# Kernel tuning notes

Hardware: AMD Instinct MI355X
Metric: run time of the kernel (lower is better)

The kernel has to match this reference:

```python
import jax, jax.numpy as jnp
import numpy as np
from jax import lax

B, T, D_IN, H1, H2 = 200, 500, 300, 256, 300


def _lstm(x, Wih, Whh, bih, bhh, H):
    """PyTorch-convention LSTM (gate order i,f,g,o), zero init state.
    x: [B,T,Din] -> outputs [B,T,H]."""
    b = x.shape[0]
    # Precompute input contribution for all timesteps: [B,T,4H]
    xg = jnp.einsum('bti,gi->btg', x, Wih) + bih + bhh

    def step(carry, xg_t):
        h, c = carry
        g = xg_t + h @ Whh.T  # [B,4H]
        i = jax.nn.sigmoid(g[:, :H])
        f = jax.nn.sigmoid(g[:, H:2 * H])
        gg = jnp.tanh(g[:, 2 * H:3 * H])
        o = jax.nn.sigmoid(g[:, 3 * H:])
        c = f * c + i * gg
        h = o * jnp.tanh(c)
        return (h, c), h

    init = (jnp.zeros((b, H), x.dtype), jnp.zeros((b, H), x.dtype))
    _, hs = lax.scan(step, init, jnp.swapaxes(xg, 0, 1))  # [T,B,H]
    return jnp.swapaxes(hs, 0, 1)


def _uniform(key, shape, H):
    s = 1.0 / np.sqrt(H)
    return jax.random.uniform(key, shape, jnp.float32, -s, s)


def setup_inputs() -> dict:
    key = jax.random.key(0)
    ks = jax.random.split(key, 10)
    x = jax.random.normal(ks[0], (B, T, D_IN), jnp.float32)
    lengths = jax.random.randint(ks[1], (B,), 1, T + 1, jnp.int32)
    return {
        'x': x,
        'lengths': lengths,
        'Wih1': _uniform(ks[2], (4 * H1, D_IN), H1),
        'Whh1': _uniform(ks[3], (4 * H1, H1), H1),
        'bih1': _uniform(ks[4], (4 * H1,), H1),
        'bhh1': _uniform(ks[5], (4 * H1,), H1),
        'Wih2': _uniform(ks[6], (4 * H2, H1), H2),
        'Whh2': _uniform(ks[7], (4 * H2, H2), H2),
        'bih2': _uniform(ks[8], (4 * H2,), H2),
        'bhh2': _uniform(ks[9], (4 * H2,), H2),
    }


def reference(x, lengths, Wih1, Whh1, bih1, bhh1, Wih2, Whh2, bih2, bhh2):
    # lstm1 on packed sequence == causal per-sample LSTM + zero out padding
    out1 = _lstm(x, Wih1, Whh1, bih1, bhh1, H1)  # [B,T,H1]
    mask = (jnp.arange(T)[None, :] < lengths[:, None])  # [B,T]
    out1 = out1 * mask[:, :, None].astype(out1.dtype)   # pad_packed zeros
    # vectorized "last valid timestep" gather (replaces host-sync loop)
    idx = (lengths - 1).astype(jnp.int32)[:, None, None]
    h_value = jnp.take_along_axis(out1, idx, axis=1)[:, 0, :]  # [B,H1]
    # lstm2 runs over the full padded (zeroed) sequence, as in the original
    out2 = _lstm(out1, Wih2, Whh2, bih2, bhh2, H2)  # [B,T,H2]
    return (out2, h_value)
```

## Files before the change

kernel.cpp:

```cpp
#include <hip/hip_runtime.h>
#include <math.h>

#define TSEQ 500
#define BQ   200
#define DIN  300
#define H1   256
#define H2   300
#define K1   556
#define KP   576
#define H1P  256
#define H2P  304
#define BQC  25
#define LB1  8
#define LBT  18
#define NBLK 144

#define H1SLOT (BQ*H1P)
#define H2SLOT (BQ*H2P)

#define WS_H1   0
#define WS_H2   307200
#define WS_C1   672000
#define WS_C2   876800
#define WS_FLG  1132800
#define WS_MSET 1133824

typedef __attribute__((ext_vector_type(8))) short short8;
typedef __attribute__((ext_vector_type(4))) float f32x4;
typedef unsigned long long u64;

__device__ __forceinline__ float sigf(float v){ return 1.0f/(1.0f+__expf(-v)); }
__device__ __forceinline__ float tanhf_(float v){
    v = fminf(15.0f, fmaxf(-15.0f, v));
    float e = __expf(2.0f*v);
    return (e-1.0f)/(e+1.0f);
}
__device__ __forceinline__ unsigned short f2bf(float f){
    unsigned int xx = __builtin_bit_cast(unsigned int, f);
    xx = (xx + 0x7FFFu + ((xx>>16)&1u)) >> 16;
    return (unsigned short)xx;
}
__device__ __forceinline__ u64 ld8_sys(const void* p){
    return __hip_atomic_load((const u64*)p, __ATOMIC_RELAXED, __HIP_MEMORY_SCOPE_SYSTEM);
}
__device__ __forceinline__ void pub8(u64* p, u64 v){
    u64 old = __hip_atomic_exchange(p, v, __ATOMIC_RELAXED, __HIP_MEMORY_SCOPE_SYSTEM);
    asm volatile("" :: "v"(old));
}

union U16B { short8 s8; u64 u[2]; unsigned short us[8]; };
union U8B  { u64 u; unsigned short us[4]; };

__global__ __launch_bounds__(512, 2)
void lstm_mfma(const float* __restrict__ x, const int* __restrict__ lengths,
               const float* __restrict__ Wih1, const float* __restrict__ Whh1,
               const float* __restrict__ bih1, const float* __restrict__ bhh1,
               const float* __restrict__ Wih2, const float* __restrict__ Whh2,
               const float* __restrict__ bih2, const float* __restrict__ bhh2,
               float* __restrict__ out, char* __restrict__ wsb,
               int it_begin, int it_end, int coop)
{
    __shared__ unsigned short Al[32*KP];
    __shared__ float gl[128*33];
    __shared__ float bias[128];
    __shared__ int lenl[32];

    const int tid = threadIdx.x;
    const int bid = blockIdx.x;
    const int mc  = bid & 7;
    const int lbi = bid >> 3;
    const bool l1 = lbi < LB1;
    const int ub  = (l1 ? lbi : lbi - LB1) * 32;
    const int Hl  = l1 ? H1 : H2;

    unsigned short* h1s = (unsigned short*)(wsb + WS_H1);
    unsigned short* h2s = (unsigned short*)(wsb + WS_H2);
    float* c1 = (float*)(wsb + WS_C1);
    float* c2 = (float*)(wsb + WS_C2);
    int* flg = (int*)(wsb + WS_FLG + mc*128);

    const int wave = tid >> 6, lane = tid & 63;
    const int fr = lane & 15, fg = lane >> 4;
    const int sw = fr & 7;

    short8 wreg[18];
    {
        const int row = wave*16 + fr;
        const int u = row >> 2, g = row & 3;
        const int unit = ub + u;
        const bool vr = unit < Hl;
        const long grow = (long)g*Hl + unit;
        #pragma unroll
        for (int ks = 0; ks < 18; ++ks){
            unsigned short v8[8];
            #pragma unroll
            for (int j = 0; j < 8; ++j){
                int k = ks*32 + fg*8 + j;
                float v = 0.0f;
                if (vr && k < K1){
                    if (l1) v = (k < H1) ? Whh1[grow*H1 + k] : Wih1[grow*DIN + (k - H1)];
                    else    v = (k < H1) ? Wih2[grow*H1 + k] : Whh2[grow*H2 + (k - H1)];
                }
                v8[j] = f2bf(v);
            }
            wreg[ks] = *(short8*)v8;
        }
    }
    if (tid < 128){
        int u = tid >> 2, g = tid & 3, unit = ub + u;
        bias[tid] = (unit < Hl)
            ? ((l1?bih1:bih2)[g*Hl+unit] + (l1?bhh1:bhh2)[g*Hl+unit]) : 0.0f;
    }
    if (tid < 32) lenl[tid] = (tid < BQC) ? lengths[mc*BQC + tid] : 0;

    const unsigned short* arow0 = &Al[fr*KP];
    const unsigned short* arow1 = &Al[(16+fr)*KP];
    const int bg_e = mc*BQC + lane;

    float creg[4] = {0.f, 0.f, 0.f, 0.f};
    if (!coop && lane < 32){
        float* cs = l1 ? c1 : c2;
        #pragma unroll
        for (int i2 = 0; i2 < 4; ++i2) creg[i2] = cs[(ub + wave*4 + i2)*BQ + bg_e];
    }

    __syncthreads();

    for (int it = it_begin; it < it_end; ++it){
        const bool active = l1 ? (it < TSEQ) : (it >= 1);
        const int t = l1 ? it : it - 1;

        if (active && l1){
            #pragma unroll
            for (int i = 0; i < 3; ++i){
                int e = tid + i*512;
                if (e < 1280){
                    int bl = e/40, kcx = 32 + e - (e/40)*40;
                    U16B v; v.u[0] = 0; v.u[1] = 0;
                    if (bl < BQC && kcx <= 69){
                        int bg = mc*BQC + bl;
                        const float* xp = x + ((size_t)bg*TSEQ + t)*DIN + (kcx*8 - 256);
                        float4 f0 = *(const float4*)xp;
                        v.us[0]=f2bf(f0.x); v.us[1]=f2bf(f0.y); v.us[2]=f2bf(f0.z); v.us[3]=f2bf(f0.w);
                        if (kcx <= 68){
                            float4 f1 = *(const float4*)(xp + 4);
                            v.us[4]=f2bf(f1.x); v.us[5]=f2bf(f1.y); v.us[6]=f2bf(f1.z); v.us[7]=f2bf(f1.w);
                        }
                    }
                    *(short8*)&Al[bl*KP + ((kcx ^ (bl&7))<<3)] = v.s8;
                }
            }
        }

        if (coop && it > it_begin && tid < LBT){
            int tgt = l1 ? (tid < LB1 ? it : it - 1) : it;
            if (tgt > 0)
                while (__hip_atomic_load(&flg[tid], __ATOMIC_RELAXED,
                                         __HIP_MEMORY_SCOPE_SYSTEM) < tgt)
                    __builtin_amdgcn_s_sleep(1);
        }
        __syncthreads();

        if (active){
            const unsigned short* h1p = h1s + (it % 3)*H1SLOT;
            const unsigned short* h2p = h2s + ((it + 2) % 3)*H2SLOT;

            f32x4 acc0 = {0.f,0.f,0.f,0.f}, acc1 = {0.f,0.f,0.f,0.f};

            if (l1){
                u64 hv0, hv1, hv2, hv3;
                const int e0 = tid, e1 = tid + 512;
                const int bl0 = e0 >> 5, kc0 = e0 & 31;
                const int bl1 = e1 >> 5, kc1 = e1 & 31;
                if (bl0 < BQC){
                    const unsigned short* hp = h1p + (size_t)(mc*BQC + bl0)*H1P + kc0*8;
                    hv0 = ld8_sys(hp); hv1 = ld8_sys(hp + 4);
                } else { hv0 = 0; hv1 = 0; }
                if (bl1 < BQC){
                    const unsigned short* hp = h1p + (size_t)(mc*BQC + bl1)*H1P + kc1*8;
                    hv2 = ld8_sys(hp); hv3 = ld8_sys(hp + 4);
                } else { hv2 = 0; hv3 = 0; }
                #pragma unroll
                for (int ks = 8; ks < 18; ++ks){
                    const int off = ((ks*4 + fg) ^ sw) << 3;
                    short8 b0 = *(const short8*)(arow0 + off);
                    short8 b1 = *(const short8*)(arow1 + off);
                    acc0 = __builtin_amdgcn_mfma_f32_16x16x32_bf16(wreg[ks], b0, acc0, 0, 0, 0);
                    acc1 = __builtin_amdgcn_mfma_f32_16x16x32_bf16(wreg[ks], b1, acc1, 0, 0, 0);
                }
                U16B w0; w0.u[0] = hv0; w0.u[1] = hv1;
                U16B w1; w1.u[0] = hv2; w1.u[1] = hv3;
                *(short8*)&Al[bl0*KP + ((kc0 ^ (bl0&7))<<3)] = w0.s8;
                *(short8*)&Al[bl1*KP + ((kc1 ^ (bl1&7))<<3)] = w1.s8;
            } else {
                u64 sv[10];
                #pragma unroll
                for (int i = 0; i < 5; ++i){
                    int e = tid + i*512;
                    u64 a = 0, b = 0;
                    if (e < 2304){
                        int bl = e/72, kc = e - (e/72)*72;
                        if (bl < BQC && kc < 70){
                            int bg = mc*BQC + bl;
                            if (kc < 32){
                                if (t < lenl[bl]){
                                    const unsigned short* hp = h1p + (size_t)bg*H1P + kc*8;
                                    a = ld8_sys(hp); b = ld8_sys(hp + 4);
                                }
                            } else {
                                const unsigned short* hp = h2p + (size_t)bg*H2P + (kc*8 - 256);
                                a = ld8_sys(hp); b = ld8_sys(hp + 4);
                            }
                        }
                    }
                    sv[2*i] = a; sv[2*i+1] = b;
                }
                #pragma unroll
                for (int i = 0; i < 5; ++i){
                    int e = tid + i*512;
                    if (e < 2304){
                        int bl = e/72, kc = e - (e/72)*72;
                        U16B v; v.u[0] = sv[2*i]; v.u[1] = sv[2*i+1];
                        *(short8*)&Al[bl*KP + ((kc ^ (bl&7))<<3)] = v.s8;
                    }
                }
            }
            __syncthreads();

            if (l1){
                #pragma unroll
                for (int ks = 0; ks < 8; ++ks){
                    const int off = ((ks*4 + fg) ^ sw) << 3;
                    short8 b0 = *(const short8*)(arow0 + off);
                    short8 b1 = *(const short8*)(arow1 + off);
                    acc0 = __builtin_amdgcn_mfma_f32_16x16x32_bf16(wreg[ks], b0, acc0, 0, 0, 0);
                    acc1 = __builtin_amdgcn_mfma_f32_16x16x32_bf16(wreg[ks], b1, acc1, 0, 0, 0);
                }
            } else {
                #pragma unroll
                for (int ks = 0; ks < 18; ++ks){
                    const int off = ((ks*4 + fg) ^ sw) << 3;
                    short8 b0 = *(const short8*)(arow0 + off);
                    short8 b1 = *(const short8*)(arow1 + off);
                    acc0 = __builtin_amdgcn_mfma_f32_16x16x32_bf16(wreg[ks], b0, acc0, 0, 0, 0);
                    acc1 = __builtin_amdgcn_mfma_f32_16x16x32_bf16(wreg[ks], b1, acc1, 0, 0, 0);
                }
            }

            const int gr = wave*16 + fg*4;
            #pragma unroll
            for (int q = 0; q < 4; ++q){
                gl[(gr+q)*33 + fr]      = acc0[q];
                gl[(gr+q)*33 + 16 + fr] = acc1[q];
            }

            if (lane < 32){
                float hv[4]; unsigned short hb[4];
                #pragma unroll
                for (int i2 = 0; i2 < 4; ++i2){
                    const int r = wave*16 + i2*4;
                    float gi = gl[(r+0)*33 + lane] + bias[r+0];
                    float gf = gl[(r+1)*33 + lane] + bias[r+1];
                    float gg = gl[(r+2)*33 + lane] + bias[r+2];
                    float go = gl[(r+3)*33 + lane] + bias[r+3];
                    float iv = sigf(gi), fv = sigf(gf), cv = tanhf_(gg), ov = sigf(go);
                    float c = fmaf(fv, creg[i2], iv*cv); creg[i2] = c;
                    hv[i2] = ov * tanhf_(c);
                    hb[i2] = f2bf(hv[i2]);
                }
                const int unit4 = ub + wave*4;
                if (lane < BQC){
                    U8B pv; pv.us[0]=hb[0]; pv.us[1]=hb[1]; pv.us[2]=hb[2]; pv.us[3]=hb[3];
                    if (l1){
                        pub8((u64*)&h1s[((it+1)%3)*H1SLOT + (size_t)bg_e*H1P + unit4], pv.u);
                        if (it == lenl[lane] - 1){
                            float4 q; q.x=hv[0]; q.y=hv[1]; q.z=hv[2]; q.w=hv[3];
                            *(float4*)(out + 30000000 + (size_t)bg_e*H1 + unit4) = q;
                        }
                    } else if (unit4 < H2){
                        pub8((u64*)&h2s[(it%3)*H2SLOT + (size_t)bg_e*H2P + unit4], pv.u);
                        float4 q; q.x=hv[0]; q.y=hv[1]; q.z=hv[2]; q.w=hv[3];
                        *(float4*)(out + (size_t)bg_e*150000 + (size_t)t*300 + unit4) = q;
                    }
                }
            }
        } else {
            __syncthreads();
        }

        __syncthreads();
        if (coop && tid == 0)
            __hip_atomic_store(&flg[lbi], it + 1, __ATOMIC_RELAXED,
                               __HIP_MEMORY_SCOPE_SYSTEM);
    }

    if (!coop && lane < 32){
        float* cs = l1 ? c1 : c2;
        #pragma unroll
        for (int i2 = 0; i2 < 4; ++i2) cs[(ub + wave*4 + i2)*BQ + bg_e] = creg[i2];
    }
}

extern "C" void kernel_launch(void* const* d_in, const int* in_sizes, int n_in,
                              void* d_out, int out_size, void* d_ws, size_t ws_size,
                              hipStream_t stream) {
    const float* x    = (const float*)d_in[0];
    const int*   lens = (const int*)  d_in[1];
    const float* Wih1 = (const float*)d_in[2];
    const float* Whh1 = (const float*)d_in[3];
    const float* bih1 = (const float*)d_in[4];
    const float* bhh1 = (const float*)d_in[5];
    const float* Wih2 = (const float*)d_in[6];
    const float* Whh2 = (const float*)d_in[7];
    const float* bih2 = (const float*)d_in[8];
    const float* bhh2 = (const float*)d_in[9];
    float* out = (float*)d_out;
    char*  ws  = (char*)d_ws;

    hipMemsetAsync(d_ws, 0, (size_t)WS_MSET, stream);

    int ib = 0, ie = TSEQ + 1, coop = 1;
    void* args[] = {(void*)&x, (void*)&lens, (void*)&Wih1, (void*)&Whh1, (void*)&bih1, (void*)&bhh1,
                    (void*)&Wih2, (void*)&Whh2, (void*)&bih2, (void*)&bhh2,
                    (void*)&out, (void*)&ws, (void*)&ib, (void*)&ie, (void*)&coop};
    hipError_t err = hipLaunchCooperativeKernel((const void*)lstm_mfma, dim3(NBLK), dim3(512),
                                                args, 0, stream);
    if (err != hipSuccess) {
        (void)hipGetLastError();
        for (int it = 0; it <= TSEQ; ++it) {
            hipLaunchKernelGGL(lstm_mfma, dim3(NBLK), dim3(512), 0, stream,
                               x, lens, Wih1, Whh1, bih1, bhh1, Wih2, Whh2, bih2, bhh2,
                               out, ws, it, it + 1, 0);
        }
    }
}
```

Measured before the change: 2.563 ms.

## Replace per-step flag barriers with poison-value dataflow sync on hidden-state buffers

Layer-1 and layer-2 blocks no longer wait on per-block progress flags before reading h. Each consumer now polls the actual hidden-state slots until they stop holding a poison sentinel, and producers re-poison the next ring slot ahead of use. Layer-1's split MFMA loop is merged into one loop, and the layer-1 flag wait for layer-2 progress moves to the end of the step. The aim is to cut inter-block synchronisation latency on the recurrent critical path. The cost is more spin traffic on system-scope loads and a correctness risk if a real bf16 pattern ever equals the poison value or the ring-slot reuse ordering is wrong.

After: 2.932 ms. 1.14x slower.

```diff
diff --git a/kernel.cpp b/kernel.cpp
--- a/kernel.cpp
+++ b/kernel.cpp
@@ -25,6 +25,8 @@
 #define WS_FLG  1132800
 #define WS_MSET 1133824
 
+#define POISON 0xFFFFFFFFFFFFFFFFull
+
 typedef __attribute__((ext_vector_type(8))) short short8;
 typedef __attribute__((ext_vector_type(4))) float f32x4;
 typedef unsigned long long u64;
@@ -50,6 +52,7 @@
 
 union U16B { short8 s8; u64 u[2]; unsigned short us[8]; };
 union U8B  { u64 u; unsigned short us[4]; };
+
 
 __global__ __launch_bounds__(512, 2)
 void lstm_mfma(const float* __restrict__ x, const int* __restrict__ lengths,
@@ -116,12 +119,13 @@
     const unsigned short* arow0 = &Al[fr*KP];
     const unsigned short* arow1 = &Al[(16+fr)*KP];
     const int bg_e = mc*BQC + lane;
+    const int unit4 = ub + wave*4;
 
     float creg[4] = {0.f, 0.f, 0.f, 0.f};
     if (!coop && lane < 32){
         float* cs = l1 ? c1 : c2;
         #pragma unroll
-        for (int i2 = 0; i2 < 4; ++i2) creg[i2] = cs[(ub + wave*4 + i2)*BQ + bg_e];
+        for (int i2 = 0; i2 < 4; ++i2) creg[i2] = cs[(unit4 + i2)*BQ + bg_e];
     }
 
     __syncthreads();
@@ -130,130 +134,140 @@
         const bool active = l1 ? (it < TSEQ) : (it >= 1);
         const int t = l1 ? it : it - 1;
 
-        if (active && l1){
-            #pragma unroll
-            for (int i = 0; i < 3; ++i){
-                int e = tid + i*512;
-                if (e < 1280){
-                    int bl = e/40, kcx = 32 + e - (e/40)*40;
-                    U16B v; v.u[0] = 0; v.u[1] = 0;
-                    if (bl < BQC && kcx <= 69){
-                        int bg = mc*BQC + bl;
-                        const float* xp = x + ((size_t)bg*TSEQ + t)*DIN + (kcx*8 - 256);
-                        float4 f0 = *(const float4*)xp;
-                        v.us[0]=f2bf(f0.x); v.us[1]=f2bf(f0.y); v.us[2]=f2bf(f0.z); v.us[3]=f2bf(f0.w);
-                        if (kcx <= 68){
-                            float4 f1 = *(const float4*)(xp + 4);
-                            v.us[4]=f2bf(f1.x); v.us[5]=f2bf(f1.y); v.us[6]=f2bf(f1.z); v.us[7]=f2bf(f1.w);
+        if (l1){
+            if (active){
+                #pragma unroll
+                for (int i = 0; i < 3; ++i){
+                    int e = tid + i*512;
+                    if (e < 1280){
+                        int bl = e/40, kcx = 32 + e - (e/40)*40;
+                        U16B v; v.u[0] = 0; v.u[1] = 0;
+                        if (bl < BQC && kcx <= 69){
+                            int bg = mc*BQC + bl;
+                            const float* xp = x + ((size_t)bg*TSEQ + t)*DIN + (kcx*8 - 256);
+                            float4 f0 = *(const float4*)xp;
+                            v.us[0]=f2bf(f0.x); v.us[1]=f2bf(f0.y); v.us[2]=f2bf(f0.z); v.us[3]=f2bf(f0.w);
+                            if (kcx <= 68){
+                                float4 f1 = *(const float4*)(xp + 4);
+                                v.us[4]=f2bf(f1.x); v.us[5]=f2bf(f1.y); v.us[6]=f2bf(f1.z); v.us[7]=f2bf(f1.w);
+                            }
                         }
-                    }
-                    *(short8*)&Al[bl*KP + ((kcx ^ (bl&7))<<3)] = v.s8;
-                }
-            }
-        }
-
-        if (coop && it > it_begin && tid < LBT){
-            int tgt = l1 ? (tid < LB1 ? it : it - 1) : it;
-            if (tgt > 0)
-                while (__hip_atomic_load(&flg[tid], __ATOMIC_RELAXED,
-                                         __HIP_MEMORY_SCOPE_SYSTEM) < tgt)
-                    __builtin_amdgcn_s_sleep(1);
-        }
-        __syncthreads();
-
-        if (active){
-            const unsigned short* h1p = h1s + (it % 3)*H1SLOT;
-            const unsigned short* h2p = h2s + ((it + 2) % 3)*H2SLOT;
-
-            f32x4 acc0 = {0.f,0.f,0.f,0.f}, acc1 = {0.f,0.f,0.f,0.f};
-
-            if (l1){
-                u64 hv0, hv1, hv2, hv3;
-                const int e0 = tid, e1 = tid + 512;
-                const int bl0 = e0 >> 5, kc0 = e0 & 31;
-                const int bl1 = e1 >> 5, kc1 = e1 & 31;
-                if (bl0 < BQC){
-                    const unsigned short* hp = h1p + (size_t)(mc*BQC + bl0)*H1P + kc0*8;
-                    hv0 = ld8_sys(hp); hv1 = ld8_sys(hp + 4);
-                } else { hv0 = 0; hv1 = 0; }
-                if (bl1 < BQC){
-                    const unsigned short* hp = h1p + (size_t)(mc*BQC + bl1)*H1P + kc1*8;
-                    hv2 = ld8_sys(hp); hv3 = ld8_sys(hp + 4);
-                } else { hv2 = 0; hv3 = 0; }
-                #pragma unroll
-                for (int ks = 8; ks < 18; ++ks){
-                    const int off = ((ks*4 + fg) ^ sw) << 3;
-                    short8 b0 = *(const short8*)(arow0 + off);
-                    short8 b1 = *(const short8*)(arow1 + off);
-                    acc0 = __builtin_amdgcn_mfma_f32_16x16x32_bf16(wreg[ks], b0, acc0, 0, 0, 0);
-                    acc1 = __builtin_amdgcn_mfma_f32_16x16x32_bf16(wreg[ks], b1, acc1, 0, 0, 0);
-                }
-                U16B w0; w0.u[0] = hv0; w0.u[1] = hv1;
-                U16B w1; w1.u[0] = hv2; w1.u[1] = hv3;
+                        *(short8*)&Al[bl*KP + ((kcx ^ (bl&7))<<3)] = v.s8;
+                    }
+                }
+                const unsigned short* h1p = h1s + (it%3)*H1SLOT;
+                const int bl0 = tid>>5, kc0 = tid&31;
+                const int bl1 = bl0 + 16;
+                u64 a0=0, a1=0, a2=0, a3=0;
+                const u64* p0 = (const u64*)(h1p + (size_t)(mc*BQC + bl0)*H1P + kc0*8);
+                const u64* p2 = (const u64*)(h1p + (size_t)(mc*BQC + bl1)*H1P + kc0*8);
+                const bool n0 = bl0 < BQC, n1 = bl1 < BQC;
+                if (coop){
+                    if (n0){ a0 = POISON; a1 = POISON; }
+                    if (n1){ a2 = POISON; a3 = POISON; }
+                    bool pend = n0 | n1;
+                    while (pend){
+                        if (a0 == POISON) a0 = ld8_sys(p0);
+                        if (a1 == POISON) a1 = ld8_sys(p0 + 1);
+                        if (a2 == POISON) a2 = ld8_sys(p2);
+                        if (a3 == POISON) a3 = ld8_sys(p2 + 1);
+                        pend = (a0==POISON)||(a1==POISON)||(a2==POISON)||(a3==POISON);
+                        if (pend) __builtin_amdgcn_s_sleep(1);
+                    }
+                } else {
+                    if (n0){ a0 = ld8_sys(p0); a1 = ld8_sys(p0 + 1); }
+                    if (n1){ a2 = ld8_sys(p2); a3 = ld8_sys(p2 + 1); }
+                }
+                U16B w0; w0.u[0] = a0; w0.u[1] = a1;
+                U16B w1; w1.u[0] = a2; w1.u[1] = a3;
                 *(short8*)&Al[bl0*KP + ((kc0 ^ (bl0&7))<<3)] = w0.s8;
-                *(short8*)&Al[bl1*KP + ((kc1 ^ (bl1&7))<<3)] = w1.s8;
-            } else {
-                u64 sv[10];
+                *(short8*)&Al[bl1*KP + ((kc0 ^ (bl1&7))<<3)] = w1.s8;
+            }
+        } else {
+            if (active){
+                const unsigned short* h1p = h1s + (it%3)*H1SLOT;
+                const unsigned short* h2p = h2s + ((it+2)%3)*H2SLOT;
+                const u64* pp[5]; bool qa[5], qb[5]; u64 va[5], vb[5];
                 #pragma unroll
                 for (int i = 0; i < 5; ++i){
-                    int e = tid + i*512;
-                    u64 a = 0, b = 0;
-                    if (e < 2304){
-                        int bl = e/72, kc = e - (e/72)*72;
-                        if (bl < BQC && kc < 70){
-                            int bg = mc*BQC + bl;
-                            if (kc < 32){
-                                if (t < lenl[bl]){
-                                    const unsigned short* hp = h1p + (size_t)bg*H1P + kc*8;
-                                    a = ld8_sys(hp); b = ld8_sys(hp + 4);
-                                }
-                            } else {
-                                const unsigned short* hp = h2p + (size_t)bg*H2P + (kc*8 - 256);
-                                a = ld8_sys(hp); b = ld8_sys(hp + 4);
+                    const int e = tid + i*512;
+                    const int bl = e/72, kc = e - (e/72)*72;
+                    pp[i] = nullptr; qa[i] = false; qb[i] = false; va[i] = 0; vb[i] = 0;
+                    if (e < 2304 && bl < BQC && kc < 70){
+                        const int bg = mc*BQC + bl;
+                        if (kc < 32){
+                            if (t < lenl[bl]){
+                                pp[i] = (const u64*)(h1p + (size_t)bg*H1P + kc*8);
+                                qa[i] = true; qb[i] = true;
                             }
+                        } else {
+                            pp[i] = (const u64*)(h2p + (size_t)bg*H2P + (kc*8 - 256));
+                            qa[i] = true; qb[i] = (kc < 69);
                         }
                     }
-                    sv[2*i] = a; sv[2*i+1] = b;
+                }
+                if (coop){
+                    #pragma unroll
+                    for (int i = 0; i < 5; ++i){ if (qa[i]) va[i] = POISON; if (qb[i]) vb[i] = POISON; }
+                    bool pend = true;
+                    while (pend){
+                        pend = false;
+                        #pragma unroll
+                        for (int i = 0; i < 5; ++i){
+                            if (qa[i] && va[i] == POISON){ va[i] = ld8_sys(pp[i]);     pend |= (va[i] == POISON); }
+                            if (qb[i] && vb[i] == POISON){ vb[i] = ld8_sys(pp[i] + 1); pend |= (vb[i] == POISON); }
+                        }
+                        if (pend) __builtin_amdgcn_s_sleep(1);
+                    }
+                } else {
+                    #pragma unroll
+                    for (int i = 0; i < 5; ++i){
+                        if (qa[i]) va[i] = ld8_sys(pp[i]);
+                        if (qb[i]) vb[i] = ld8_sys(pp[i] + 1);
+                    }
                 }
                 #pragma unroll
                 for (int i = 0; i < 5; ++i){
-                    int e = tid + i*512;
+                    const int e = tid + i*512;
                     if (e < 2304){
-                        int bl = e/72, kc = e - (e/72)*72;
-                        U16B v; v.u[0] = sv[2*i]; v.u[1] = sv[2*i+1];
+                        const int bl = e/72, kc = e - (e/72)*72;
+                        U16B v; v.u[0] = va[i]; v.u[1] = vb[i];
                         *(short8*)&Al[bl*KP + ((kc ^ (bl&7))<<3)] = v.s8;
                     }
                 }
             }
-            __syncthreads();
-
+        }
+
+        __syncthreads();
+        if (!l1 && coop && tid == 0)
+            __hip_atomic_store(&flg[lbi], it + 1, __ATOMIC_RELAXED,
+                               __HIP_MEMORY_SCOPE_SYSTEM);
+
+        if (coop && lane < BQC){
             if (l1){
-                #pragma unroll
-                for (int ks = 0; ks < 8; ++ks){
-                    const int off = ((ks*4 + fg) ^ sw) << 3;
-                    short8 b0 = *(const short8*)(arow0 + off);
-                    short8 b1 = *(const short8*)(arow1 + off);
-                    acc0 = __builtin_amdgcn_mfma_f32_16x16x32_bf16(wreg[ks], b0, acc0, 0, 0, 0);
-                    acc1 = __builtin_amdgcn_mfma_f32_16x16x32_bf16(wreg[ks], b1, acc1, 0, 0, 0);
-                }
-            } else {
-                #pragma unroll
-                for (int ks = 0; ks < 18; ++ks){
-                    const int off = ((ks*4 + fg) ^ sw) << 3;
-                    short8 b0 = *(const short8*)(arow0 + off);
-                    short8 b1 = *(const short8*)(arow1 + off);
-                    acc0 = __builtin_amdgcn_mfma_f32_16x16x32_bf16(wreg[ks], b0, acc0, 0, 0, 0);
-                    acc1 = __builtin_amdgcn_mfma_f32_16x16x32_bf16(wreg[ks], b1, acc1, 0, 0, 0);
-                }
-            }
-
+                if (it + 1 < TSEQ)
+                    pub8((u64*)&h1s[((it+2)%3)*H1SLOT + (size_t)bg_e*H1P + unit4], POISON);
+            } else if (unit4 < H2){
+                pub8((u64*)&h2s[((it+1)%3)*H2SLOT + (size_t)bg_e*H2P + unit4], POISON);
+            }
+        }
+
+        if (active){
+            f32x4 acc0 = {0.f,0.f,0.f,0.f}, acc1 = {0.f,0.f,0.f,0.f};
+            #pragma unroll
+            for (int ks = 0; ks < 18; ++ks){
+                const int off = ((ks*4 + fg) ^ sw) << 3;
+                short8 b0 = *(const short8*)(arow0 + off);
+                short8 b1 = *(const short8*)(arow1 + off);
+                acc0 = __builtin_amdgcn_mfma_f32_16x16x32_bf16(wreg[ks], b0, acc0, 0, 0, 0);
+                acc1 = __builtin_amdgcn_mfma_f32_16x16x32_bf16(wreg[ks], b1, acc1, 0, 0, 0);
+            }
             const int gr = wave*16 + fg*4;
             #pragma unroll
             for (int q = 0; q < 4; ++q){
                 gl[(gr+q)*33 + fr]      = acc0[q];
                 gl[(gr+q)*33 + 16 + fr] = acc1[q];
             }
-
             if (lane < 32){
                 float hv[4]; unsigned short hb[4];
                 #pragma unroll
@@ -268,7 +282,6 @@
                     hv[i2] = ov * tanhf_(c);
                     hb[i2] = f2bf(hv[i2]);
                 }
-                const int unit4 = ub + wave*4;
                 if (lane < BQC){
                     U8B pv; pv.us[0]=hb[0]; pv.us[1]=hb[1]; pv.us[2]=hb[2]; pv.us[3]=hb[3];
                     if (l1){
@@ -284,20 +297,24 @@
                     }
                 }
             }
-        } else {
-            __syncthreads();
-        }
-
-        __syncthreads();
-        if (coop && tid == 0)
-            __hip_atomic_store(&flg[lbi], it + 1, __ATOMIC_RELAXED,
-                               __HIP_MEMORY_SCOPE_SYSTEM);
+        }
+
+        if (l1 && coop && (it + 1 < it_end) && tid < 10){
+            while (__hip_atomic_load(&flg[8 + tid], __ATOMIC_RELAXED,
+                                     __HIP_MEMORY_SCOPE_SYSTEM) < it + 1)
+                __builtin_amdgcn_s_sleep(1);
+        }
+
+        asm volatile("s_waitcnt lgkmcnt(0)" ::: "memory");
+        __builtin_amdgcn_sched_barrier(0);
+        __builtin_amdgcn_s_barrier();
+        __builtin_amdgcn_sched_barrier(0);
     }
 
     if (!coop && lane < 32){
         float* cs = l1 ? c1 : c2;
         #pragma unroll
-        for (int i2 = 0; i2 < 4; ++i2) cs[(ub + wave*4 + i2)*BQ + bg_e] = creg[i2];
+        for (int i2 = 0; i2 < 4; ++i2) cs[(unit4 + i2)*BQ + bg_e] = creg[i2];
     }
 }
 
@@ -318,6 +335,8 @@
     char*  ws  = (char*)d_ws;
 
     hipMemsetAsync(d_ws, 0, (size_t)WS_MSET, stream);
+    hipMemsetAsync(ws + WS_H1 + H1SLOT*2 , 0xFF,
+                   (size_t)H1SLOT*2, stream);
 
     int ib = 0, ie = TSEQ + 1, coop = 1;
     void* args[] = {(void*)&x, (void*)&lens, (void*)&Wih1, (void*)&Whh1, (void*)&bih1, (void*)&bhh1,
```

## Narrow atomic scope to agent and make layer-1 waits per-thread and finer-grained

Applied to the files above, without the earlier changes.

Switches the h-state loads, publish exchanges and flag accesses from system scope to agent scope, so they skip system-coherence handling. In layer 1, each thread now waits only on the flag of the producer block that owns its h chunk, instead of a few threads waiting on all flags before a barrier. The wait for layer-2 consumers (a WAR guard on the ring slot) moves after the loads. The split MFMA loop that overlapped the x-part with the h load is replaced by a single 18-step loop after the barrier, which drops that overlap in exchange for the finer-grained waiting.

Result: faster. 2.505 ms (-2.2%).

```diff
diff --git a/kernel.cpp b/kernel.cpp
--- a/kernel.cpp
+++ b/kernel.cpp
@@ -40,16 +40,23 @@
     xx = (xx + 0x7FFFu + ((xx>>16)&1u)) >> 16;
     return (unsigned short)xx;
 }
-__device__ __forceinline__ u64 ld8_sys(const void* p){
-    return __hip_atomic_load((const u64*)p, __ATOMIC_RELAXED, __HIP_MEMORY_SCOPE_SYSTEM);
+__device__ __forceinline__ u64 ld8c(const void* p){
+    return __hip_atomic_load((const u64*)p, __ATOMIC_RELAXED, __HIP_MEMORY_SCOPE_AGENT);
 }
 __device__ __forceinline__ void pub8(u64* p, u64 v){
-    u64 old = __hip_atomic_exchange(p, v, __ATOMIC_RELAXED, __HIP_MEMORY_SCOPE_SYSTEM);
+    u64 old = __hip_atomic_exchange(p, v, __ATOMIC_RELAXED, __HIP_MEMORY_SCOPE_AGENT);
     asm volatile("" :: "v"(old));
+}
+__device__ __forceinline__ int ldflag(const int* p){
+    return __hip_atomic_load(p, __ATOMIC_RELAXED, __HIP_MEMORY_SCOPE_AGENT);
+}
+__device__ __forceinline__ void stflag(int* p, int v){
+    __hip_atomic_store(p, v, __ATOMIC_RELAXED, __HIP_MEMORY_SCOPE_AGENT);
 }
 
 union U16B { short8 s8; u64 u[2]; unsigned short us[8]; };
 union U8B  { u64 u; unsigned short us[4]; };
+
 
 __global__ __launch_bounds__(512, 2)
 void lstm_mfma(const float* __restrict__ x, const int* __restrict__ lengths,
@@ -116,12 +123,13 @@
     const unsigned short* arow0 = &Al[fr*KP];
     const unsigned short* arow1 = &Al[(16+fr)*KP];
     const int bg_e = mc*BQC + lane;
+    const int unit4 = ub + wave*4;
 
     float creg[4] = {0.f, 0.f, 0.f, 0.f};
     if (!coop && lane < 32){
         float* cs = l1 ? c1 : c2;
         #pragma unroll
-        for (int i2 = 0; i2 < 4; ++i2) creg[i2] = cs[(ub + wave*4 + i2)*BQ + bg_e];
+        for (int i2 = 0; i2 < 4; ++i2) creg[i2] = cs[(unit4 + i2)*BQ + bg_e];
     }
 
     __syncthreads();
@@ -130,69 +138,62 @@
         const bool active = l1 ? (it < TSEQ) : (it >= 1);
         const int t = l1 ? it : it - 1;
 
-        if (active && l1){
-            #pragma unroll
-            for (int i = 0; i < 3; ++i){
-                int e = tid + i*512;
-                if (e < 1280){
-                    int bl = e/40, kcx = 32 + e - (e/40)*40;
-                    U16B v; v.u[0] = 0; v.u[1] = 0;
-                    if (bl < BQC && kcx <= 69){
-                        int bg = mc*BQC + bl;
-                        const float* xp = x + ((size_t)bg*TSEQ + t)*DIN + (kcx*8 - 256);
-                        float4 f0 = *(const float4*)xp;
-                        v.us[0]=f2bf(f0.x); v.us[1]=f2bf(f0.y); v.us[2]=f2bf(f0.z); v.us[3]=f2bf(f0.w);
-                        if (kcx <= 68){
-                            float4 f1 = *(const float4*)(xp + 4);
-                            v.us[4]=f2bf(f1.x); v.us[5]=f2bf(f1.y); v.us[6]=f2bf(f1.z); v.us[7]=f2bf(f1.w);
+        if (l1){
+            if (active){
+                #pragma unroll
+                for (int i = 0; i < 3; ++i){
+                    int e = tid + i*512;
+                    if (e < 1280){
+                        int bl = e/40, kcx = 32 + e - (e/40)*40;
+                        U16B v; v.u[0] = 0; v.u[1] = 0;
+                        if (bl < BQC && kcx <= 69){
+                            int bg = mc*BQC + bl;
+                            const float* xp = x + ((size_t)bg*TSEQ + t)*DIN + (kcx*8 - 256);
+                            float4 f0 = *(const float4*)xp;
+                            v.us[0]=f2bf(f0.x); v.us[1]=f2bf(f0.y); v.us[2]=f2bf(f0.z); v.us[3]=f2bf(f0.w);
+                            if (kcx <= 68){
+                                float4 f1 = *(const float4*)(xp + 4);
+                                v.us[4]=f2bf(f1.x); v.us[5]=f2bf(f1.y); v.us[6]=f2bf(f1.z); v.us[7]=f2bf(f1.w);
+                            }
                         }
+                        *(short8*)&Al[bl*KP + ((kcx ^ (bl&7))<<3)] = v.s8;
                     }
-                    *(short8*)&Al[bl*KP + ((kcx ^ (bl&7))<<3)] = v.s8;
-                }
-            }
-        }
-
-        if (coop && it > it_begin && tid < LBT){
-            int tgt = l1 ? (tid < LB1 ? it : it - 1) : it;
-            if (tgt > 0)
-                while (__hip_atomic_load(&flg[tid], __ATOMIC_RELAXED,
-                                         __HIP_MEMORY_SCOPE_SYSTEM) < tgt)
-                    __builtin_amdgcn_s_sleep(1);
-        }
-        __syncthreads();
-
-        if (active){
-            const unsigned short* h1p = h1s + (it % 3)*H1SLOT;
-            const unsigned short* h2p = h2s + ((it + 2) % 3)*H2SLOT;
-
-            f32x4 acc0 = {0.f,0.f,0.f,0.f}, acc1 = {0.f,0.f,0.f,0.f};
-
-            if (l1){
-                u64 hv0, hv1, hv2, hv3;
-                const int e0 = tid, e1 = tid + 512;
-                const int bl0 = e0 >> 5, kc0 = e0 & 31;
-                const int bl1 = e1 >> 5, kc1 = e1 & 31;
-                if (bl0 < BQC){
+                }
+                const int kc0 = tid & 31;
+                const int bl0 = tid >> 5, bl1 = bl0 + 16;
+                if (coop && it > it_begin){
+                    const int* fp = &flg[kc0 >> 2];
+                    while (ldflag(fp) < it) __builtin_amdgcn_s_sleep(1);
+                    asm volatile("" ::: "memory");
+                }
+                const unsigned short* h1p = h1s + (it % 3)*H1SLOT;
+                u64 a0, a1, a2 = 0, a3 = 0;
+                {
                     const unsigned short* hp = h1p + (size_t)(mc*BQC + bl0)*H1P + kc0*8;
-                    hv0 = ld8_sys(hp); hv1 = ld8_sys(hp + 4);
-                } else { hv0 = 0; hv1 = 0; }
+                    a0 = ld8c(hp); a1 = ld8c(hp + 4);
+                }
                 if (bl1 < BQC){
-                    const unsigned short* hp = h1p + (size_t)(mc*BQC + bl1)*H1P + kc1*8;
-                    hv2 = ld8_sys(hp); hv3 = ld8_sys(hp + 4);
-                } else { hv2 = 0; hv3 = 0; }
-                #pragma unroll
-                for (int ks = 8; ks < 18; ++ks){
-                    const int off = ((ks*4 + fg) ^ sw) << 3;
-                    short8 b0 = *(const short8*)(arow0 + off);
-                    short8 b1 = *(const short8*)(arow1 + off);
-                    acc0 = __builtin_amdgcn_mfma_f32_16x16x32_bf16(wreg[ks], b0, acc0, 0, 0, 0);
-                    acc1 = __builtin_amdgcn_mfma_f32_16x16x32_bf16(wreg[ks], b1, acc1, 0, 0, 0);
-                }
-                U16B w0; w0.u[0] = hv0; w0.u[1] = hv1;
-                U16B w1; w1.u[0] = hv2; w1.u[1] = hv3;
+                    const unsigned short* hp = h1p + (size_t)(mc*BQC + bl1)*H1P + kc0*8;
+                    a2 = ld8c(hp); a3 = ld8c(hp + 4);
+                }
+                U16B w0; w0.u[0] = a0; w0.u[1] = a1;
+                U16B w1; w1.u[0] = a2; w1.u[1] = a3;
                 *(short8*)&Al[bl0*KP + ((kc0 ^ (bl0&7))<<3)] = w0.s8;
-                *(short8*)&Al[bl1*KP + ((kc1 ^ (bl1&7))<<3)] = w1.s8;
-            } else {
+                *(short8*)&Al[bl1*KP + ((kc0 ^ (bl1&7))<<3)] = w1.s8;
+                if (coop && tid < 10 && it >= 2){
+                    while (ldflag(&flg[8 + tid]) < it - 1) __builtin_amdgcn_s_sleep(1);
+                }
+            }
+        } else {
+            if (coop && it > it_begin && tid < LBT){
+                if (active){
+                    while (ldflag(&flg[tid]) < it) __builtin_amdgcn_s_sleep(1);
+                }
+            }
+            __syncthreads();
+            if (active){
+                const unsigned short* h1p = h1s + (it % 3)*H1SLOT;
+                const unsigned short* h2p = h2s + ((it + 2) % 3)*H2SLOT;
                 u64 sv[10];
                 #pragma unroll
                 for (int i = 0; i < 5; ++i){
@@ -205,11 +206,11 @@
                             if (kc < 32){
                                 if (t < lenl[bl]){
                                     const unsigned short* hp = h1p + (size_t)bg*H1P + kc*8;
-                                    a = ld8_sys(hp); b = ld8_sys(hp + 4);
+                                    a = ld8c(hp); b = ld8c(hp + 4);
                                 }
                             } else {
                                 const unsigned short* hp = h2p + (size_t)bg*H2P + (kc*8 - 256);
-                                a = ld8_sys(hp); b = ld8_sys(hp + 4);
+                                a = ld8c(hp); b = ld8c(hp + 4);
                             }
                         }
                     }
@@ -225,35 +226,25 @@
                     }
                 }
             }
-            __syncthreads();
-
-            if (l1){
-                #pragma unroll
-                for (int ks = 0; ks < 8; ++ks){
-                    const int off = ((ks*4 + fg) ^ sw) << 3;
-                    short8 b0 = *(const short8*)(arow0 + off);
-                    short8 b1 = *(const short8*)(arow1 + off);
-                    acc0 = __builtin_amdgcn_mfma_f32_16x16x32_bf16(wreg[ks], b0, acc0, 0, 0, 0);
-                    acc1 = __builtin_amdgcn_mfma_f32_16x16x32_bf16(wreg[ks], b1, acc1, 0, 0, 0);
-                }
-            } else {
-                #pragma unroll
-                for (int ks = 0; ks < 18; ++ks){
-                    const int off = ((ks*4 + fg) ^ sw) << 3;
-                    short8 b0 = *(const short8*)(arow0 + off);
-                    short8 b1 = *(const short8*)(arow1 + off);
-                    acc0 = __builtin_amdgcn_mfma_f32_16x16x32_bf16(wreg[ks], b0, acc0, 0, 0, 0);
-                    acc1 = __builtin_amdgcn_mfma_f32_16x16x32_bf16(wreg[ks], b1, acc1, 0, 0, 0);
-                }
-            }
-
+        }
+        __syncthreads();
+
+        if (active){
+            f32x4 acc0 = {0.f,0.f,0.f,0.f}, acc1 = {0.f,0.f,0.f,0.f};
+            #pragma unroll
+            for (int ks = 0; ks < 18; ++ks){
+                const int off = ((ks*4 + fg) ^ sw) << 3;
+                short8 b0 = *(const short8*)(arow0 + off);
+                short8 b1 = *(const short8*)(arow1 + off);
+                acc0 = __builtin_amdgcn_mfma_f32_16x16x32_bf16(wreg[ks], b0, acc0, 0, 0, 0);
+                acc1 = __builtin_amdgcn_mfma_f32_16x16x32_bf16(wreg[ks], b1, acc1, 0, 0, 0);
+            }
             const int gr = wave*16 + fg*4;
             #pragma unroll
             for (int q = 0; q < 4; ++q){
                 gl[(gr+q)*33 + fr]      = acc0[q];
                 gl[(gr+q)*33 + 16 + fr] = acc1[q];
             }
-
             if (lane < 32){
                 float hv[4]; unsigned short hb[4];
                 #pragma unroll
@@ -268,7 +259,6 @@
                     hv[i2] = ov * tanhf_(c);
                     hb[i2] = f2bf(hv[i2]);
                 }
-                const int unit4 = ub + wave*4;
                 if (lane < BQC){
                     U8B pv; pv.us[0]=hb[0]; pv.us[1]=hb[1]; pv.us[2]=hb[2]; pv.us[3]=hb[3];
                     if (l1){
@@ -284,20 +274,17 @@
                     }
                 }
             }
-        } else {
-            __syncthreads();
         }
 
         __syncthreads();
         if (coop && tid == 0)
-            __hip_atomic_store(&flg[lbi], it + 1, __ATOMIC_RELAXED,
-                               __HIP_MEMORY_SCOPE_SYSTEM);
+            stflag(&flg[lbi], it + 1);
     }
 
     if (!coop && lane < 32){
         float* cs = l1 ? c1 : c2;
         #pragma unroll
-        for (int i2 = 0; i2 < 4; ++i2) cs[(ub + wave*4 + i2)*BQ + bg_e] = creg[i2];
+        for (int i2 = 0; i2 < 4; ++i2) cs[(unit4 + i2)*BQ + bg_e] = creg[i2];
     }
 }
 
```
